# Kernel optimization log

Measured on AMD Instinct MI355X. Metric: run time of the kernel, lower is better.

The kernel has to match this reference:

```python
import jax, jax.numpy as jnp
import numpy as np

HIDDEN = 1024
HEADS = 16
CHUNK = 128
NEG_INF = -1e10  # matches source's -10000000000.0


def setup_inputs() -> dict:
    key = jax.random.key(0)
    k1, k2, k3 = jax.random.split(key, 3)
    B, S = 2, 4096
    x = jax.random.normal(k1, (B, S, HIDDEN), dtype=jnp.float32)
    w_qkv = jax.random.normal(k2, (HIDDEN, 3 * HIDDEN), dtype=jnp.float32) / np.sqrt(HIDDEN).astype(np.float32)
    w_out = jax.random.normal(k3, (HIDDEN, HIDDEN), dtype=jnp.float32) / np.sqrt(HIDDEN).astype(np.float32)
    return {"x": x, "w_qkv": w_qkv, "w_out": w_out}


def reference(x, w_qkv, w_out):
    B, S, _ = x.shape
    H, D = HEADS, HIDDEN // HEADS
    # fused qkv projection (flax Dense, no bias): [B,S,3,H,D]
    qkv = (x @ w_qkv).reshape(B, S, 3, H, D)
    q, k, v = qkv[:, :, 0], qkv[:, :, 1], qkv[:, :, 2]
    scale = jnp.sqrt(jnp.asarray(D, x.dtype))
    n_chunks = S // CHUNK
    # [n_chunks, B, CHUNK, H, D] query chunks; scan keeps only one chunk's
    # [B,H,CHUNK,S] score tensor live at a time (faithful to source's chunking).
    q_chunks = q.reshape(B, n_chunks, CHUNK, H, D).transpose(1, 0, 2, 3, 4)
    starts = jnp.arange(n_chunks) * CHUNK

    def step(carry, inp):
        qc, start = inp  # qc: [B,CHUNK,H,D]
        scores = jnp.einsum('bqhd,bkhd->bhqk', qc, k) / scale  # [B,H,CHUNK,S]
        causal = (jnp.arange(CHUNK)[:, None] + start) >= jnp.arange(S)[None, :]
        scores = jnp.where(causal[None, None], scores, NEG_INF)
        attn = jax.nn.softmax(scores, axis=-1)
        out_c = jnp.einsum('bhqk,bkhd->bqhd', attn, v).reshape(B, CHUNK, H * D)
        return carry, out_c

    _, outs = jax.lax.scan(step, None, (q_chunks, starts))  # [n,B,CHUNK,hidden]
    out = outs.transpose(1, 0, 2, 3).reshape(B, S, H * D)
    return out @ w_out
```

## Files before the change

kernel.cpp:

```cpp
#include <hip/hip_runtime.h>
#include <hip/hip_bf16.h>

#define SEQ 4096
#define BATCH 2
#define HEADS 16
#define DHEAD 64
#define HID 1024

typedef unsigned short ushort_t;
typedef __attribute__((ext_vector_type(8))) short short8;
typedef __attribute__((ext_vector_type(4))) float f32x4;

__device__ __forceinline__ float exp2_fast(float x) {
  return __builtin_amdgcn_exp2f(x);
}

__device__ __forceinline__ ushort_t f2b(float f) {
  unsigned u = __builtin_bit_cast(unsigned, f);
  unsigned r = 0x7fffu + ((u >> 16) & 1u);
  return (ushort_t)((u + r) >> 16);
}

__device__ __forceinline__ unsigned cvt_pk_bf16(float lo, float hi) {
  unsigned r;
  asm("v_cvt_pk_bf16_f32 %0, %1, %2" : "=v"(r) : "v"(lo), "v"(hi));
  return r;
}

__device__ __forceinline__ void gload16(const void* g, void* l) {
  __builtin_amdgcn_global_load_lds((const __attribute__((address_space(1))) void*)g,
                                   (__attribute__((address_space(3))) void*)l, 16, 0, 0);
}

__device__ __forceinline__ f32x4 mfma_bf16(short8 a, short8 b, f32x4 c) {
  return __builtin_amdgcn_mfma_f32_16x16x32_bf16(a, b, c, 0, 0, 0);
}

__global__ void cvt_kernel(const float* __restrict__ in, ushort_t* __restrict__ out, int n4) {
  int i = blockIdx.x * blockDim.x + threadIdx.x;
  if (i >= n4) return;
  float4 v = reinterpret_cast<const float4*>(in)[i];
  ushort4 o;
  o.x = f2b(v.x); o.y = f2b(v.y); o.z = f2b(v.z); o.w = f2b(v.w);
  reinterpret_cast<ushort4*>(out)[i] = o;
}

__global__ void transpose_cvt_kernel(const float* __restrict__ in, ushort_t* __restrict__ out,
                                     int rows, int cols) {
  __shared__ float tile[32][33];
  int tx = threadIdx.x & 31, ty = threadIdx.x >> 5;
  int r0 = blockIdx.y * 32, c0 = blockIdx.x * 32;
#pragma unroll
  for (int i = 0; i < 32; i += 8)
    tile[ty + i][tx] = in[(size_t)(r0 + ty + i) * cols + c0 + tx];
  __syncthreads();
#pragma unroll
  for (int i = 0; i < 32; i += 8)
    out[(size_t)(c0 + ty + i) * rows + r0 + tx] = f2b(tile[tx][ty + i]);
}

template <int MODE>
__global__ __launch_bounds__(256, 2)
void gemm_kernel(const ushort_t* __restrict__ A, const ushort_t* __restrict__ BT,
                 int M, int N, int K,
                 ushort_t* __restrict__ qg, ushort_t* __restrict__ kg,
                 ushort_t* __restrict__ vTg, float* __restrict__ outf) {
  __shared__ ushort_t lA[128 * 64];
  __shared__ ushort_t lB[128 * 64];
  int tid = threadIdx.x;
  int lane = tid & 63, w = tid >> 6;
  int m0 = blockIdx.x * 128, n0 = blockIdx.y * 128;
  int wr = (w >> 1) * 64, wc = (w & 1) * 64;
  int lr = lane & 15, lg = lane >> 4;

  const f32x4 z4 = {0.f, 0.f, 0.f, 0.f};
  f32x4 acc[4][4];
#pragma unroll
  for (int m = 0; m < 4; ++m)
#pragma unroll
    for (int n = 0; n < 4; ++n) acc[m][n] = z4;

  int ktiles = K >> 6;
  for (int kt = 0; kt < ktiles; ++kt) {
    int k0 = kt << 6;
#pragma unroll
    for (int i = 0; i < 4; ++i) {
      int c = i * 256 + tid;
      int row = c >> 3, cc = c & 7;
      gload16(A + (size_t)(m0 + row) * K + k0 + (cc ^ (row & 7)) * 8, lA + c * 8);
    }
#pragma unroll
    for (int i = 0; i < 4; ++i) {
      int c = i * 256 + tid;
      int row = c >> 3, cc = c & 7;
      gload16(BT + (size_t)(n0 + row) * K + k0 + (cc ^ (row & 7)) * 8, lB + c * 8);
    }
    __syncthreads();
#pragma unroll
    for (int kk = 0; kk < 2; ++kk) {
      short8 a[4], b[4];
#pragma unroll
      for (int m = 0; m < 4; ++m) {
        int row = wr + m * 16 + lr, cc = kk * 4 + lg;
        a[m] = *(const short8*)(lA + row * 64 + ((cc ^ (row & 7)) << 3));
      }
#pragma unroll
      for (int n = 0; n < 4; ++n) {
        int row = wc + n * 16 + lr, cc = kk * 4 + lg;
        b[n] = *(const short8*)(lB + row * 64 + ((cc ^ (row & 7)) << 3));
      }
      __builtin_amdgcn_s_setprio(1);
#pragma unroll
      for (int m = 0; m < 4; ++m)
#pragma unroll
        for (int n = 0; n < 4; ++n)
          acc[m][n] = mfma_bf16(a[m], b[n], acc[m][n]);
      __builtin_amdgcn_s_setprio(0);
    }
    __syncthreads();
  }

#pragma unroll
  for (int m = 0; m < 4; ++m)
#pragma unroll
    for (int n = 0; n < 4; ++n)
#pragma unroll
      for (int r = 0; r < 4; ++r) {
        int i = m0 + wr + m * 16 + lg * 4 + r;
        int j = n0 + wc + n * 16 + lr;
        float v = acc[m][n][r];
        if (MODE == 0) {
          int mat = j >> 10, rem = j & 1023;
          int h = rem >> 6, d = rem & 63;
          int b = i >> 12, s = i & 4095;
          int bh = b * HEADS + h;
          ushort_t val = f2b(mat == 0 ? v * 0.18033688f : v);
          if (mat == 0)      qg[((size_t)bh * SEQ + s) * DHEAD + d] = val;
          else if (mat == 1) kg[((size_t)bh * SEQ + s) * DHEAD + d] = val;
          else               vTg[((size_t)bh * DHEAD + d) * SEQ + s] = val;
        } else {
          outf[(size_t)i * N + j] = v;
        }
      }
}

struct QState {
  short8 qf[2][2];
  float mrow[2], lsum[2];
  f32x4 o[2][4];
};

__device__ __forceinline__ void attn_tile(int jt, int qt, int w, int lr, int lg, int lane,
                                          const ushort_t* lK, const ushort_t* lV,
                                          ushort_t* lP, QState& st) {
  const f32x4 z4 = {0.f, 0.f, 0.f, 0.f};
  f32x4 s[2][8];
#pragma unroll
  for (int qm = 0; qm < 2; ++qm)
#pragma unroll
    for (int kt = 0; kt < 8; ++kt) s[qm][kt] = z4;
#pragma unroll
  for (int kk = 0; kk < 2; ++kk) {
#pragma unroll
    for (int kt = 0; kt < 8; ++kt) {
      int row = kt * 16 + lr;
      short8 kf = *(const short8*)(lK + row * 64 + (((kk * 4 + lg) ^ (row & 7)) << 3));
      __builtin_amdgcn_s_setprio(1);
      s[0][kt] = mfma_bf16(kf, st.qf[0][kk], s[0][kt]);
      s[1][kt] = mfma_bf16(kf, st.qf[1][kk], s[1][kt]);
      __builtin_amdgcn_s_setprio(0);
    }
  }

  if (jt == qt) {
#pragma unroll
    for (int qm = 0; qm < 2; ++qm) {
      int qgl = w * 32 + qm * 16 + lr;
#pragma unroll
      for (int kt = 0; kt < 8; ++kt)
#pragma unroll
        for (int r = 0; r < 4; ++r)
          if (kt * 16 + lg * 4 + r > qgl) s[qm][kt][r] = -1e30f;
    }
  }

  float alv[2] = {1.f, 1.f};
  int resc = 0;
#pragma unroll
  for (int qm = 0; qm < 2; ++qm) {
    float mx = s[qm][0][0];
#pragma unroll
    for (int kt = 0; kt < 8; ++kt)
#pragma unroll
      for (int r = 0; r < 4; ++r) mx = fmaxf(mx, s[qm][kt][r]);
    mx = fmaxf(mx, __shfl_xor(mx, 16));
    mx = fmaxf(mx, __shfl_xor(mx, 32));
    float mo = st.mrow[qm];
    if (!__all(mx - mo <= 8.0f)) {
      float mn = fmaxf(mo, mx);
      float al = exp2_fast(mo - mn);
      st.mrow[qm] = mn;
      st.lsum[qm] *= al;
      alv[qm] = al;
      resc |= (1 << qm);
    }
    float mloc = st.mrow[qm];
    float rs = 0.f;
#pragma unroll
    for (int kt = 0; kt < 8; ++kt)
#pragma unroll
      for (int r = 0; r < 4; ++r) {
        float p = exp2_fast(s[qm][kt][r] - mloc);
        s[qm][kt][r] = p;
        rs += p;
      }
    rs += __shfl_xor(rs, 16);
    rs += __shfl_xor(rs, 32);
    st.lsum[qm] += rs;
  }
  if (resc) {
#pragma unroll
    for (int m = 0; m < 2; ++m)
      if (resc & (1 << m)) {
#pragma unroll
        for (int r = 0; r < 4; ++r) {
          float alo = __shfl(alv[m], (lane & 48) | (lg * 4 + r));
#pragma unroll
          for (int nd = 0; nd < 4; ++nd) st.o[m][nd][r] *= alo;
        }
      }
  }

#pragma unroll
  for (int qm = 0; qm < 2; ++qm) {
    int q = w * 32 + qm * 16 + lr;
#pragma unroll
    for (int kt = 0; kt < 8; ++kt) {
      uint2 pw;
      pw.x = cvt_pk_bf16(s[qm][kt][0], s[qm][kt][1]);
      pw.y = cvt_pk_bf16(s[qm][kt][2], s[qm][kt][3]);
      int c = kt * 2 + (lg >> 1);
      *(uint2*)(lP + q * 128 + (((c ^ (q & 15)) << 3) | ((lg & 1) << 2))) = pw;
    }
  }

#pragma unroll
  for (int kk = 0; kk < 4; ++kk) {
    short8 a[2];
#pragma unroll
    for (int m = 0; m < 2; ++m) {
      int q = w * 32 + m * 16 + lr;
      a[m] = *(const short8*)(lP + q * 128 + (((kk * 4 + lg) ^ (q & 15)) << 3));
    }
#pragma unroll
    for (int nd = 0; nd < 4; ++nd) {
      int row = nd * 16 + lr;
      short8 b = *(const short8*)(lV + row * 128 + (((kk * 4 + lg) ^ (row & 15)) << 3));
      __builtin_amdgcn_s_setprio(1);
      st.o[0][nd] = mfma_bf16(a[0], b, st.o[0][nd]);
      st.o[1][nd] = mfma_bf16(a[1], b, st.o[1][nd]);
      __builtin_amdgcn_s_setprio(0);
    }
  }
}

__device__ __forceinline__ void attn_epilogue(const QState& st, int q0, int bh,
                                              int w, int lr, int lg, int lane,
                                              ushort_t* __restrict__ og) {
  int b = bh >> 4, h = bh & 15;
#pragma unroll
  for (int m = 0; m < 2; ++m)
#pragma unroll
    for (int r = 0; r < 4; ++r) {
      float ls = __shfl(st.lsum[m], (lane & 48) | (lg * 4 + r));
      float inv = 1.0f / ls;
      int srow = q0 + w * 32 + m * 16 + lg * 4 + r;
#pragma unroll
      for (int nd = 0; nd < 4; ++nd) {
        int col = h * 64 + nd * 16 + lr;
        og[((size_t)b * SEQ + srow) * HID + col] = f2b(st.o[m][nd][r] * inv);
      }
    }
}

__global__ __launch_bounds__(256, 2)
void attn_kernel(const ushort_t* __restrict__ qg, const ushort_t* __restrict__ kg,
                 const ushort_t* __restrict__ vTg, ushort_t* __restrict__ og) {
  __shared__ ushort_t lK[128 * 64];
  __shared__ ushort_t lV[64 * 128];
  __shared__ ushort_t lP[128 * 128];

  int bid = blockIdx.x;
  int wg = (bid & 7) * 64 + (bid >> 3);
  int bh = wg >> 4;
  int pair = wg & 15;
  int qtA = 31 - pair, qtB = pair;
  int q0A = qtA * 128, q0B = qtB * 128;
  const ushort_t* Q = qg + (size_t)bh * SEQ * DHEAD;
  const ushort_t* Kp = kg + (size_t)bh * SEQ * DHEAD;
  const ushort_t* Vt = vTg + (size_t)bh * DHEAD * SEQ;

  int tid = threadIdx.x, lane = tid & 63, w = tid >> 6;
  int lr = lane & 15, lg = lane >> 4;

#pragma unroll
  for (int i = 0; i < 4; ++i) {
    int c = i * 256 + tid;
    int row = c >> 3, cc = c & 7;
    gload16(Q + (size_t)(q0A + row) * DHEAD + (cc ^ (row & 7)) * 8, lP + c * 8);
    gload16(Q + (size_t)(q0B + row) * DHEAD + (cc ^ (row & 7)) * 8, lP + 8192 + c * 8);
  }
  __syncthreads();
  QState stA, stB;
#pragma unroll
  for (int qm = 0; qm < 2; ++qm)
#pragma unroll
    for (int kk = 0; kk < 2; ++kk) {
      int row = w * 32 + qm * 16 + lr;
      int off = row * 64 + (((kk * 4 + lg) ^ (row & 7)) << 3);
      stA.qf[qm][kk] = *(const short8*)(lP + off);
      stB.qf[qm][kk] = *(const short8*)(lP + 8192 + off);
    }
  asm volatile("s_waitcnt lgkmcnt(0)");

  const f32x4 z4 = {0.f, 0.f, 0.f, 0.f};
#pragma unroll
  for (int qm = 0; qm < 2; ++qm) {
    stA.mrow[qm] = -1e30f; stA.lsum[qm] = 0.f;
    stB.mrow[qm] = -1e30f; stB.lsum[qm] = 0.f;
#pragma unroll
    for (int n = 0; n < 4; ++n) { stA.o[qm][n] = z4; stB.o[qm][n] = z4; }
  }

  for (int jt = 0; jt <= qtA; ++jt) {
    int j0 = jt * 128;
#pragma unroll
    for (int i = 0; i < 4; ++i) {
      int c = i * 256 + tid;
      int row = c >> 3, cc = c & 7;
      gload16(Kp + (size_t)(j0 + row) * DHEAD + (cc ^ (row & 7)) * 8, lK + c * 8);
    }
#pragma unroll
    for (int i = 0; i < 4; ++i) {
      int c = i * 256 + tid;
      int d = c >> 4, cc = c & 15;
      gload16(Vt + (size_t)d * SEQ + j0 + (cc ^ (d & 15)) * 8, lV + c * 8);
    }
    __syncthreads();

    attn_tile(jt, qtA, w, lr, lg, lane, lK, lV, lP, stA);
    if (jt <= qtB) attn_tile(jt, qtB, w, lr, lg, lane, lK, lV, lP, stB);

    __syncthreads();
  }

  attn_epilogue(stA, q0A, bh, w, lr, lg, lane, og);
  attn_epilogue(stB, q0B, bh, w, lr, lg, lane, og);
}

extern "C" void kernel_launch(void* const* d_in, const int* in_sizes, int n_in,
                              void* d_out, int out_size, void* d_ws, size_t ws_size,
                              hipStream_t stream) {
  const float* x = (const float*)d_in[0];
  const float* wqkv = (const float*)d_in[1];
  const float* wout = (const float*)d_in[2];
  float* out = (float*)d_out;

  if (ws_size < 75497472u) return;

  char* ws = (char*)d_ws;
  ushort_t* xb    = (ushort_t*)(ws);
  ushort_t* wqkvT = (ushort_t*)(ws + 16777216);
  ushort_t* woutT = (ushort_t*)(ws + 23068672);
  ushort_t* qgb   = (ushort_t*)(ws + 25165824);
  ushort_t* kgb   = (ushort_t*)(ws + 41943040);
  ushort_t* vTb   = (ushort_t*)(ws + 58720256);
  ushort_t* ob    = xb;

  cvt_kernel<<<dim3(8192), dim3(256), 0, stream>>>(x, xb, 2097152);
  transpose_cvt_kernel<<<dim3(96, 32), dim3(256), 0, stream>>>(wqkv, wqkvT, 1024, 3072);
  transpose_cvt_kernel<<<dim3(32, 32), dim3(256), 0, stream>>>(wout, woutT, 1024, 1024);
  gemm_kernel<0><<<dim3(64, 24), dim3(256), 0, stream>>>(xb, wqkvT, 8192, 3072, 1024,
                                                         qgb, kgb, vTb, nullptr);
  attn_kernel<<<dim3(512), dim3(256), 0, stream>>>(qgb, kgb, vTb, ob);
  gemm_kernel<1><<<dim3(64, 8), dim3(256), 0, stream>>>(ob, woutT, 8192, 1024, 1024,
                                                        nullptr, nullptr, nullptr, out);
}
```

Measured before the change: 229.2 us.

## Double-buffer K/V tiles, hoist V fragments to registers, shrink P scratch

Prefetches the next K and V tiles into a second LDS buffer while the current tile is computed, so global loads overlap with MFMA work and the per-tile barrier before compute goes away. V operand fragments are now read from LDS once per key tile into registers and shared by both query tiles. The P scratch buffer is cut to 16 rows per wave and reused for each qm half, with the rescale folded inline. This costs about 64 extra VGPRs per thread, which risks spilling or lower occupancy, and it doubles the K/V LDS footprint.

```diff
diff --git a/kernel.cpp b/kernel.cpp
--- a/kernel.cpp
+++ b/kernel.cpp
@@ -151,7 +151,7 @@
 };
 
 __device__ __forceinline__ void attn_tile(int jt, int qt, int w, int lr, int lg, int lane,
-                                          const ushort_t* lK, const ushort_t* lV,
+                                          const ushort_t* lKc, const short8 (&bv)[4][4],
                                           ushort_t* lP, QState& st) {
   const f32x4 z4 = {0.f, 0.f, 0.f, 0.f};
   f32x4 s[2][8];
@@ -164,7 +164,7 @@
 #pragma unroll
     for (int kt = 0; kt < 8; ++kt) {
       int row = kt * 16 + lr;
-      short8 kf = *(const short8*)(lK + row * 64 + (((kk * 4 + lg) ^ (row & 7)) << 3));
+      short8 kf = *(const short8*)(lKc + row * 64 + (((kk * 4 + lg) ^ (row & 7)) << 3));
       __builtin_amdgcn_s_setprio(1);
       s[0][kt] = mfma_bf16(kf, st.qf[0][kk], s[0][kt]);
       s[1][kt] = mfma_bf16(kf, st.qf[1][kk], s[1][kt]);
@@ -184,8 +184,7 @@
     }
   }
 
-  float alv[2] = {1.f, 1.f};
-  int resc = 0;
+  int slot = w * 16 + lr;
 #pragma unroll
   for (int qm = 0; qm < 2; ++qm) {
     float mx = s[qm][0][0];
@@ -201,8 +200,12 @@
       float al = exp2_fast(mo - mn);
       st.mrow[qm] = mn;
       st.lsum[qm] *= al;
-      alv[qm] = al;
-      resc |= (1 << qm);
+#pragma unroll
+      for (int r = 0; r < 4; ++r) {
+        float alo = __shfl(al, (lane & 48) | (lg * 4 + r));
+#pragma unroll
+        for (int nd = 0; nd < 4; ++nd) st.o[qm][nd][r] *= alo;
+      }
     }
     float mloc = st.mrow[qm];
     float rs = 0.f;
@@ -217,48 +220,23 @@
     rs += __shfl_xor(rs, 16);
     rs += __shfl_xor(rs, 32);
     st.lsum[qm] += rs;
-  }
-  if (resc) {
-#pragma unroll
-    for (int m = 0; m < 2; ++m)
-      if (resc & (1 << m)) {
-#pragma unroll
-        for (int r = 0; r < 4; ++r) {
-          float alo = __shfl(alv[m], (lane & 48) | (lg * 4 + r));
-#pragma unroll
-          for (int nd = 0; nd < 4; ++nd) st.o[m][nd][r] *= alo;
-        }
-      }
-  }
-
-#pragma unroll
-  for (int qm = 0; qm < 2; ++qm) {
-    int q = w * 32 + qm * 16 + lr;
+
 #pragma unroll
     for (int kt = 0; kt < 8; ++kt) {
       uint2 pw;
       pw.x = cvt_pk_bf16(s[qm][kt][0], s[qm][kt][1]);
       pw.y = cvt_pk_bf16(s[qm][kt][2], s[qm][kt][3]);
       int c = kt * 2 + (lg >> 1);
-      *(uint2*)(lP + q * 128 + (((c ^ (q & 15)) << 3) | ((lg & 1) << 2))) = pw;
-    }
-  }
-
-#pragma unroll
-  for (int kk = 0; kk < 4; ++kk) {
-    short8 a[2];
-#pragma unroll
-    for (int m = 0; m < 2; ++m) {
-      int q = w * 32 + m * 16 + lr;
-      a[m] = *(const short8*)(lP + q * 128 + (((kk * 4 + lg) ^ (q & 15)) << 3));
-    }
-#pragma unroll
-    for (int nd = 0; nd < 4; ++nd) {
-      int row = nd * 16 + lr;
-      short8 b = *(const short8*)(lV + row * 128 + (((kk * 4 + lg) ^ (row & 15)) << 3));
+      *(uint2*)(lP + slot * 128 + (((c ^ lr) << 3) | ((lg & 1) << 2))) = pw;
+    }
+
+#pragma unroll
+    for (int kk = 0; kk < 4; ++kk) {
+      short8 a = *(const short8*)(lP + slot * 128 + (((kk * 4 + lg) ^ lr) << 3));
       __builtin_amdgcn_s_setprio(1);
-      st.o[0][nd] = mfma_bf16(a[0], b, st.o[0][nd]);
-      st.o[1][nd] = mfma_bf16(a[1], b, st.o[1][nd]);
+#pragma unroll
+      for (int nd = 0; nd < 4; ++nd)
+        st.o[qm][nd] = mfma_bf16(a, bv[kk][nd], st.o[qm][nd]);
       __builtin_amdgcn_s_setprio(0);
     }
   }
@@ -286,9 +264,9 @@
 __global__ __launch_bounds__(256, 2)
 void attn_kernel(const ushort_t* __restrict__ qg, const ushort_t* __restrict__ kg,
                  const ushort_t* __restrict__ vTg, ushort_t* __restrict__ og) {
-  __shared__ ushort_t lK[128 * 64];
-  __shared__ ushort_t lV[64 * 128];
-  __shared__ ushort_t lP[128 * 128];
+  __shared__ ushort_t lK[2][128 * 64];
+  __shared__ ushort_t lV[2][64 * 128];
+  __shared__ ushort_t lP[64 * 128];
 
   int bid = blockIdx.x;
   int wg = (bid & 7) * 64 + (bid >> 3);
@@ -307,10 +285,19 @@
   for (int i = 0; i < 4; ++i) {
     int c = i * 256 + tid;
     int row = c >> 3, cc = c & 7;
-    gload16(Q + (size_t)(q0A + row) * DHEAD + (cc ^ (row & 7)) * 8, lP + c * 8);
-    gload16(Q + (size_t)(q0B + row) * DHEAD + (cc ^ (row & 7)) * 8, lP + 8192 + c * 8);
+    size_t qoff = (cc ^ (row & 7)) * 8;
+    gload16(Q + (size_t)(q0A + row) * DHEAD + qoff, &lK[1][c * 8]);
+    gload16(Q + (size_t)(q0B + row) * DHEAD + qoff, &lV[1][c * 8]);
+    gload16(Kp + (size_t)row * DHEAD + qoff, &lK[0][c * 8]);
+  }
+#pragma unroll
+  for (int i = 0; i < 4; ++i) {
+    int c = i * 256 + tid;
+    int d = c >> 4, cc = c & 15;
+    gload16(Vt + (size_t)d * SEQ + (cc ^ (d & 15)) * 8, &lV[0][c * 8]);
   }
   __syncthreads();
+
   QState stA, stB;
 #pragma unroll
   for (int qm = 0; qm < 2; ++qm)
@@ -318,10 +305,11 @@
     for (int kk = 0; kk < 2; ++kk) {
       int row = w * 32 + qm * 16 + lr;
       int off = row * 64 + (((kk * 4 + lg) ^ (row & 7)) << 3);
-      stA.qf[qm][kk] = *(const short8*)(lP + off);
-      stB.qf[qm][kk] = *(const short8*)(lP + 8192 + off);
+      stA.qf[qm][kk] = *(const short8*)(&lK[1][0] + off);
+      stB.qf[qm][kk] = *(const short8*)(&lV[1][0] + off);
     }
   asm volatile("s_waitcnt lgkmcnt(0)");
+  __syncthreads();
 
   const f32x4 z4 = {0.f, 0.f, 0.f, 0.f};
 #pragma unroll
@@ -333,23 +321,34 @@
   }
 
   for (int jt = 0; jt <= qtA; ++jt) {
-    int j0 = jt * 128;
-#pragma unroll
-    for (int i = 0; i < 4; ++i) {
-      int c = i * 256 + tid;
-      int row = c >> 3, cc = c & 7;
-      gload16(Kp + (size_t)(j0 + row) * DHEAD + (cc ^ (row & 7)) * 8, lK + c * 8);
-    }
-#pragma unroll
-    for (int i = 0; i < 4; ++i) {
-      int c = i * 256 + tid;
-      int d = c >> 4, cc = c & 15;
-      gload16(Vt + (size_t)d * SEQ + j0 + (cc ^ (d & 15)) * 8, lV + c * 8);
-    }
-    __syncthreads();
-
-    attn_tile(jt, qtA, w, lr, lg, lane, lK, lV, lP, stA);
-    if (jt <= qtB) attn_tile(jt, qtB, w, lr, lg, lane, lK, lV, lP, stB);
+    int cur = jt & 1, nxt = cur ^ 1;
+    if (jt < qtA) {
+      int j0n = (jt + 1) * 128;
+#pragma unroll
+      for (int i = 0; i < 4; ++i) {
+        int c = i * 256 + tid;
+        int row = c >> 3, cc = c & 7;
+        gload16(Kp + (size_t)(j0n + row) * DHEAD + (cc ^ (row & 7)) * 8, &lK[nxt][c * 8]);
+      }
+#pragma unroll
+      for (int i = 0; i < 4; ++i) {
+        int c = i * 256 + tid;
+        int d = c >> 4, cc = c & 15;
+        gload16(Vt + (size_t)d * SEQ + j0n + (cc ^ (d & 15)) * 8, &lV[nxt][c * 8]);
+      }
+    }
+
+    short8 bv[4][4];
+#pragma unroll
+    for (int kk = 0; kk < 4; ++kk)
+#pragma unroll
+      for (int nd = 0; nd < 4; ++nd) {
+        int row = nd * 16 + lr;
+        bv[kk][nd] = *(const short8*)(&lV[cur][0] + row * 128 + (((kk * 4 + lg) ^ (row & 15)) << 3));
+      }
+
+    attn_tile(jt, qtA, w, lr, lg, lane, &lK[cur][0], bv, lP, stA);
+    if (jt <= qtB) attn_tile(jt, qtB, w, lr, lg, lane, &lK[cur][0], bv, lP, stB);
 
     __syncthreads();
   }
```

Result: slower. 311.9 us (+36.1%).
